# Optimization experiments

Measured on AMD Instinct MI355X. Metric: run time of the kernel, lower is better.

## Reference

```python
import jax, jax.numpy as jnp
import numpy as np

LEVELS = 3  # num_basis = 1 + 1 + 2 + 4 = 8


def _haar_basis(x):
    """Closed-form vectorized Haar basis, x: [B, F] raw inputs.

    Replaces the original nested per-feature/per-level/per-bucket mask loops:
    at each level only one bucket k = floor(u*freq) is active, with value
    +2^(level/2) on the left half of the bucket and -2^(level/2) on the right
    half (x == 1.0 falls in the right half of the last bucket, matching the
    torch edge-case handling).
    """
    u = (jnp.tanh(x) + 1.0) / 2.0  # normalize to [0, 1]
    cols = [jnp.ones_like(u)[..., None]]  # scaling function phi
    for level in range(LEVELS):
        freq = 2 ** level
        k = jnp.clip(jnp.floor(u * freq), 0, freq - 1).astype(jnp.int32)  # bucket idx
        mid = (k.astype(u.dtype) + 0.5) / freq
        amp = jnp.asarray(2.0 ** (level / 2), u.dtype)
        sign = jnp.where(u < mid, amp, -amp)  # [B, F]
        cols.append(jax.nn.one_hot(k, freq, dtype=u.dtype) * sign[..., None])
    return jnp.concatenate(cols, axis=-1)  # [B, F, num_basis]


def setup_inputs() -> dict:
    key = jax.random.key(0)
    k1, k2, k3 = jax.random.split(key, 3)
    B, F, O, NB = 32768, 1024, 64, 8
    x = jax.random.normal(k1, (B, F), dtype=jnp.float32)
    coeffs = jax.random.normal(k2, (F, O, NB), dtype=jnp.float32) * 0.05
    base_weight = jax.random.normal(k3, (F, O), dtype=jnp.float32) * 0.05
    return {"x": x, "coeffs": coeffs, "base_weight": base_weight}


def reference(x, coeffs, base_weight):
    basis = _haar_basis(x)                         # [B, F, NB]
    wave_out = jnp.einsum('bin,ion->bo', basis, coeffs)  # [B, O]
    out = wave_out + x @ base_weight               # residual path
    kl = jnp.zeros((1,), dtype=x.dtype)            # non-variational: kl = 0
    return (out, kl)
```

## Files before the change

### kernel.cpp

```cpp
#include <hip/hip_runtime.h>
#include <math.h>


typedef __attribute__((ext_vector_type(8))) short short8;
typedef __attribute__((ext_vector_type(4))) float f32x4;

__device__ __forceinline__ unsigned int f2bf(float f) {
  unsigned int u = __float_as_uint(f);
  u += 0x7FFFu + ((u >> 16) & 1u);
  return u >> 16;
}

__device__ __forceinline__ void gen_basis(int j, unsigned int* d) {
  d[0] = (j < 4) ? 0x3F803F80u : 0xBF803F80u;
  unsigned int sq1 = (j & 2) ? 0xBFB5u : 0x3FB5u;
  d[1] = (j & 4) ? (sq1 << 16) : sq1;
  unsigned long long sd2 = (j & 1) ? 0xC000ull : 0x4000ull;
  unsigned long long d23 = sd2 << ((j & 6) << 3);
  d[2] = (unsigned int)d23;
  d[3] = (unsigned int)(d23 >> 32);
}

#define BARRIER() __asm__ volatile("s_waitcnt lgkmcnt(0)\n\ts_barrier" ::: "memory")

__device__ __forceinline__ void build_chunk(const float4& xa, const float4& xb,
                                            uint4* __restrict__ dst) {
  float xv[8];
  xv[0] = xa.x; xv[1] = xa.y; xv[2] = xa.z; xv[3] = xa.w;
  xv[4] = xb.x; xv[5] = xb.y; xv[6] = xb.z; xv[7] = xb.w;
  float t8v[8];
  unsigned int bad = 0;
#pragma unroll
  for (int ff = 0; ff < 8; ++ff) {
    float e = __expf(2.0f * xv[ff]);
    float r = __builtin_amdgcn_rcpf(e + 1.0f);
    float t8 = __builtin_fmaf(-8.0f, r, 8.0f);
    float rn = rintf(t8);
    if (fabsf(t8 - rn) < 3e-5f) bad |= 1u << ff;
    t8v[ff] = t8;
  }
  if (__builtin_expect(bad != 0, 0)) {
#pragma unroll
    for (int ff = 0; ff < 8; ++ff)
      if (bad & (1u << ff)) {
        float tf = (float)tanh((double)xv[ff]);
        t8v[ff] = ((tf + 1.0f) * 0.5f) * 8.0f;
      }
  }
  unsigned int dw[36];
#pragma unroll
  for (int p = 0; p < 4; ++p) {
    int je = (int)t8v[2 * p];     je = je > 7 ? 7 : je;
    int jo = (int)t8v[2 * p + 1]; jo = jo > 7 ? 7 : jo;
    gen_basis(je, &dw[9 * p]);
    dw[9 * p + 4] = f2bf(xv[2 * p]) | (f2bf(xv[2 * p + 1]) << 16);
    gen_basis(jo, &dw[9 * p + 5]);
  }
#pragma unroll
  for (int gg = 0; gg < 9; ++gg) {
    uint4 qv; qv.x = dw[4 * gg]; qv.y = dw[4 * gg + 1];
    qv.z = dw[4 * gg + 2]; qv.w = dw[4 * gg + 3];
    dst[gg * 256] = qv;
  }
}

__global__ __launch_bounds__(256) void build_w(const float* __restrict__ coeffs,
                                               const float* __restrict__ bw,
                                               uint4* __restrict__ Wsw) {
  const int l = threadIdx.x & 63;
  const int t = threadIdx.x >> 6;
  const int g = blockIdx.x;
  const int c = g / 9, j = g - c * 9;
  const int R = c * 4 + (l >> 4);
  const int o = t * 16 + (l & 15);
  unsigned int dwv[4];
#pragma unroll
  for (int jj = 0; jj < 8; ++jj) {
    int d = 8 * j + jj;
    int p = d / 18;
    int e = d - p * 18;
    int f, n;
    if (e < 8)       { f = 8 * R + 2 * p;     n = e; }
    else if (e == 8) { f = 8 * R + 2 * p;     n = 8; }
    else if (e == 9) { f = 8 * R + 2 * p + 1; n = 8; }
    else             { f = 8 * R + 2 * p + 1; n = e - 10; }
    float v = (n < 8) ? coeffs[(f * 64 + o) * 8 + n] : bw[f * 64 + o];
    unsigned int h = f2bf(v);
    if (jj & 1) dwv[jj >> 1] |= h << 16; else dwv[jj >> 1] = h;
  }
  uint4 qq; qq.x = dwv[0]; qq.y = dwv[1]; qq.z = dwv[2]; qq.w = dwv[3];
  Wsw[(g * 4 + t) * 64 + l] = qq;
}

template <int NS>
__device__ __forceinline__ void run_main(const float* __restrict__ xrow,
                                         const uint4* __restrict__ Wsw,
                                         uint4* __restrict__ Albuf,
                                         f32x4* acc,
                                         int s0, int q, int mm, int bdoff, int l) {
  float4 xa = *(const float4*)(xrow);
  float4 xb = *(const float4*)(xrow + 4);
  build_chunk(xa, xb, Albuf + bdoff);
  xa = *(const float4*)(xrow + 32);
  xb = *(const float4*)(xrow + 36);
  BARRIER();
  for (int c = 0; c < 32; ++c) {
    uint4* cur = Albuf + (c & 1) * 2304;
    uint4* nxt = Albuf + ((c + 1) & 1) * 2304;
    uint4 Bv[NS][4];
#pragma unroll
    for (int i = 0; i < NS; ++i) {
      const uint4* wp = Wsw + (size_t)((c * 9 + s0 + 4 * i) * 256) + l;
      Bv[i][0] = wp[0]; Bv[i][1] = wp[64]; Bv[i][2] = wp[128]; Bv[i][3] = wp[192];
    }
    if (c + 1 < 32) {
      build_chunk(xa, xb, nxt + bdoff);
      if (c + 2 < 32) {
        xa = *(const float4*)(xrow + (c + 2) * 32);
        xb = *(const float4*)(xrow + (c + 2) * 32 + 4);
      }
    }
#pragma unroll
    for (int i = 0; i < NS; ++i) {
      const int sl = s0 + 4 * i;
      const uint4* rb = cur + sl * 256 + q * 64 + mm;
      short8 a0 = __builtin_bit_cast(short8, rb[0]);
      short8 a1 = __builtin_bit_cast(short8, rb[16]);
      short8 a2 = __builtin_bit_cast(short8, rb[32]);
      short8 a3 = __builtin_bit_cast(short8, rb[48]);
#pragma unroll
      for (int t = 0; t < 4; ++t) {
        short8 Bt = __builtin_bit_cast(short8, Bv[i][t]);
        acc[0 * 4 + t] = __builtin_amdgcn_mfma_f32_16x16x32_bf16(a0, Bt, acc[0 * 4 + t], 0, 0, 0);
        acc[1 * 4 + t] = __builtin_amdgcn_mfma_f32_16x16x32_bf16(a1, Bt, acc[1 * 4 + t], 0, 0, 0);
        acc[2 * 4 + t] = __builtin_amdgcn_mfma_f32_16x16x32_bf16(a2, Bt, acc[2 * 4 + t], 0, 0, 0);
        acc[3 * 4 + t] = __builtin_amdgcn_mfma_f32_16x16x32_bf16(a3, Bt, acc[3 * 4 + t], 0, 0, 0);
      }
    }
    BARRIER();
  }
}

__global__ __launch_bounds__(256, 2) void wavelet_gemm(const float* __restrict__ x,
                                                       const uint4* __restrict__ Wsw,
                                                       float* __restrict__ out,
                                                       int out_size) {
  __shared__ uint4 Albuf[2 * 9 * 4 * 64];
  const int tid = threadIdx.x;
  const int l = tid & 63;
  const int w = tid >> 6;
  const int q = l >> 4;
  const int mm = l & 15;
  const int m = tid & 63;
  const int bdoff = w * 64 + m;
  const long rowbase = (long)blockIdx.x * 64;

  f32x4 acc[16];
#pragma unroll
  for (int i = 0; i < 16; ++i) acc[i] = (f32x4){0.f, 0.f, 0.f, 0.f};

  const float* xrow = x + (rowbase + m) * 1024 + w * 8;

  if (w == 0) run_main<3>(xrow, Wsw, Albuf, acc, 0, q, mm, bdoff, l);
  else        run_main<2>(xrow, Wsw, Albuf, acc, w, q, mm, bdoff, l);

  float* P = (float*)Albuf;
  float* W = P + w * 4096;
#pragma unroll
  for (int rt = 0; rt < 4; ++rt)
#pragma unroll
    for (int tt = 0; tt < 4; ++tt)
      *(f32x4*)(W + (16 * tt + mm) * 64 + 16 * rt + 4 * q) = acc[rt * 4 + tt];
  BARRIER();

  const int col = tid & 63;
  float* og = out + (size_t)rowbase * 64;
#pragma unroll
  for (int s = 0; s < 4; ++s) {
    int rg = s * 4 + (tid >> 6);
    f32x4 v = *(f32x4*)(P + 0 * 4096 + col * 64 + 4 * rg);
    v = v + *(f32x4*)(P + 1 * 4096 + col * 64 + 4 * rg);
    v = v + *(f32x4*)(P + 2 * 4096 + col * 64 + 4 * rg);
    v = v + *(f32x4*)(P + 3 * 4096 + col * 64 + 4 * rg);
#pragma unroll
    for (int r = 0; r < 4; ++r)
      og[(4 * rg + r) * 64 + col] = v[r];
  }
  if (blockIdx.x == 0 && tid == 0) out[out_size - 1] = 0.0f;
}

extern "C" void kernel_launch(void* const* d_in, const int* in_sizes, int n_in,
                              void* d_out, int out_size, void* d_ws, size_t ws_size,
                              hipStream_t stream) {
  const float* x      = (const float*)d_in[0];
  const float* coeffs = (const float*)d_in[1];
  const float* bw     = (const float*)d_in[2];
  uint4* Wsw = (uint4*)d_ws;
  float* out = (float*)d_out;

  build_w<<<288, 256, 0, stream>>>(coeffs, bw, Wsw);
  wavelet_gemm<<<512, 256, 0, stream>>>(x, (const uint4*)Wsw, out, out_size);
}
```

Measured before the change: 231.7 us.

## Split GEMM tile across 8 waves by output quadrant, dropping split-K LDS reduction

The main kernel now uses 512 threads (8 waves). Each wave owns a 32-row by 16-column output tile and covers the full K range, instead of 4 waves splitting K and reducing partial sums through shared memory. Basis building is halved per thread, so each thread encodes 4 features, and results are written directly from accumulators. This removes the LDS reduction and the heavy per-wave accumulator state, at the cost of each wave loading all 9 B slices per chunk and issuing fewer MFMAs per A load.

```diff
diff --git a/kernel.cpp b/kernel.cpp
--- a/kernel.cpp
+++ b/kernel.cpp
@@ -23,15 +23,13 @@
 
 #define BARRIER() __asm__ volatile("s_waitcnt lgkmcnt(0)\n\ts_barrier" ::: "memory")
 
-__device__ __forceinline__ void build_chunk(const float4& xa, const float4& xb,
-                                            uint4* __restrict__ dst) {
-  float xv[8];
-  xv[0] = xa.x; xv[1] = xa.y; xv[2] = xa.z; xv[3] = xa.w;
-  xv[4] = xb.x; xv[5] = xb.y; xv[6] = xb.z; xv[7] = xb.w;
-  float t8v[8];
+__device__ __forceinline__ void build_half(const float4& xq,
+                                           uint4* __restrict__ dst, int h) {
+  float xv[4] = {xq.x, xq.y, xq.z, xq.w};
+  float t8v[4];
   unsigned int bad = 0;
 #pragma unroll
-  for (int ff = 0; ff < 8; ++ff) {
+  for (int ff = 0; ff < 4; ++ff) {
     float e = __expf(2.0f * xv[ff]);
     float r = __builtin_amdgcn_rcpf(e + 1.0f);
     float t8 = __builtin_fmaf(-8.0f, r, 8.0f);
@@ -41,27 +39,34 @@
   }
   if (__builtin_expect(bad != 0, 0)) {
 #pragma unroll
-    for (int ff = 0; ff < 8; ++ff)
+    for (int ff = 0; ff < 4; ++ff)
       if (bad & (1u << ff)) {
         float tf = (float)tanh((double)xv[ff]);
         t8v[ff] = ((tf + 1.0f) * 0.5f) * 8.0f;
       }
   }
-  unsigned int dw[36];
+  unsigned int dw[18];
 #pragma unroll
-  for (int p = 0; p < 4; ++p) {
+  for (int p = 0; p < 2; ++p) {
     int je = (int)t8v[2 * p];     je = je > 7 ? 7 : je;
     int jo = (int)t8v[2 * p + 1]; jo = jo > 7 ? 7 : jo;
     gen_basis(je, &dw[9 * p]);
     dw[9 * p + 4] = f2bf(xv[2 * p]) | (f2bf(xv[2 * p + 1]) << 16);
     gen_basis(jo, &dw[9 * p + 5]);
   }
+  const int db = h ? 2 : 0;
+  const int gb = h ? 5 : 0;
 #pragma unroll
-  for (int gg = 0; gg < 9; ++gg) {
-    uint4 qv; qv.x = dw[4 * gg]; qv.y = dw[4 * gg + 1];
-    qv.z = dw[4 * gg + 2]; qv.w = dw[4 * gg + 3];
-    dst[gg * 256] = qv;
+  for (int k = 0; k < 4; ++k) {
+    uint4 qv;
+    qv.x = dw[db + 4 * k];     qv.y = dw[db + 4 * k + 1];
+    qv.z = dw[db + 4 * k + 2]; qv.w = dw[db + 4 * k + 3];
+    dst[(gb + k) * 256] = qv;
   }
+  uint2 hv;
+  if (h) { hv.x = dw[0];  hv.y = dw[1];  }
+  else   { hv.x = dw[16]; hv.y = dw[17]; }
+  ((uint2*)(dst + 4 * 256))[h] = hv;
 }
 
 __global__ __launch_bounds__(256) void build_w(const float* __restrict__ coeffs,
@@ -85,107 +90,73 @@
     else if (e == 9) { f = 8 * R + 2 * p + 1; n = 8; }
     else             { f = 8 * R + 2 * p + 1; n = e - 10; }
     float v = (n < 8) ? coeffs[(f * 64 + o) * 8 + n] : bw[f * 64 + o];
-    unsigned int h = f2bf(v);
-    if (jj & 1) dwv[jj >> 1] |= h << 16; else dwv[jj >> 1] = h;
+    unsigned int hh = f2bf(v);
+    if (jj & 1) dwv[jj >> 1] |= hh << 16; else dwv[jj >> 1] = hh;
   }
   uint4 qq; qq.x = dwv[0]; qq.y = dwv[1]; qq.z = dwv[2]; qq.w = dwv[3];
   Wsw[(g * 4 + t) * 64 + l] = qq;
 }
 
-template <int NS>
-__device__ __forceinline__ void run_main(const float* __restrict__ xrow,
-                                         const uint4* __restrict__ Wsw,
-                                         uint4* __restrict__ Albuf,
-                                         f32x4* acc,
-                                         int s0, int q, int mm, int bdoff, int l) {
-  float4 xa = *(const float4*)(xrow);
-  float4 xb = *(const float4*)(xrow + 4);
-  build_chunk(xa, xb, Albuf + bdoff);
-  xa = *(const float4*)(xrow + 32);
-  xb = *(const float4*)(xrow + 36);
-  BARRIER();
-  for (int c = 0; c < 32; ++c) {
-    uint4* cur = Albuf + (c & 1) * 2304;
-    uint4* nxt = Albuf + ((c + 1) & 1) * 2304;
-    uint4 Bv[NS][4];
-#pragma unroll
-    for (int i = 0; i < NS; ++i) {
-      const uint4* wp = Wsw + (size_t)((c * 9 + s0 + 4 * i) * 256) + l;
-      Bv[i][0] = wp[0]; Bv[i][1] = wp[64]; Bv[i][2] = wp[128]; Bv[i][3] = wp[192];
-    }
-    if (c + 1 < 32) {
-      build_chunk(xa, xb, nxt + bdoff);
-      if (c + 2 < 32) {
-        xa = *(const float4*)(xrow + (c + 2) * 32);
-        xb = *(const float4*)(xrow + (c + 2) * 32 + 4);
-      }
-    }
-#pragma unroll
-    for (int i = 0; i < NS; ++i) {
-      const int sl = s0 + 4 * i;
-      const uint4* rb = cur + sl * 256 + q * 64 + mm;
-      short8 a0 = __builtin_bit_cast(short8, rb[0]);
-      short8 a1 = __builtin_bit_cast(short8, rb[16]);
-      short8 a2 = __builtin_bit_cast(short8, rb[32]);
-      short8 a3 = __builtin_bit_cast(short8, rb[48]);
-#pragma unroll
-      for (int t = 0; t < 4; ++t) {
-        short8 Bt = __builtin_bit_cast(short8, Bv[i][t]);
-        acc[0 * 4 + t] = __builtin_amdgcn_mfma_f32_16x16x32_bf16(a0, Bt, acc[0 * 4 + t], 0, 0, 0);
-        acc[1 * 4 + t] = __builtin_amdgcn_mfma_f32_16x16x32_bf16(a1, Bt, acc[1 * 4 + t], 0, 0, 0);
-        acc[2 * 4 + t] = __builtin_amdgcn_mfma_f32_16x16x32_bf16(a2, Bt, acc[2 * 4 + t], 0, 0, 0);
-        acc[3 * 4 + t] = __builtin_amdgcn_mfma_f32_16x16x32_bf16(a3, Bt, acc[3 * 4 + t], 0, 0, 0);
-      }
-    }
-    BARRIER();
-  }
-}
-
-__global__ __launch_bounds__(256, 2) void wavelet_gemm(const float* __restrict__ x,
+__global__ __launch_bounds__(512, 4) void wavelet_gemm(const float* __restrict__ x,
                                                        const uint4* __restrict__ Wsw,
                                                        float* __restrict__ out,
                                                        int out_size) {
-  __shared__ uint4 Albuf[2 * 9 * 4 * 64];
+  __shared__ uint4 Albuf[2 * 9 * 256];
   const int tid = threadIdx.x;
   const int l = tid & 63;
   const int w = tid >> 6;
   const int q = l >> 4;
   const int mm = l & 15;
-  const int m = tid & 63;
-  const int bdoff = w * 64 + m;
+  const int mh = w >> 2;
+  const int nq = w & 3;
+  const int r = w & 3;
+  const int h = w >> 2;
+  const int m = l;
   const long rowbase = (long)blockIdx.x * 64;
 
-  f32x4 acc[16];
-#pragma unroll
-  for (int i = 0; i < 16; ++i) acc[i] = (f32x4){0.f, 0.f, 0.f, 0.f};
+  const int wr_off  = r * 64 + m;
+  const int rd_base = q * 64 + mh * 32 + mm;
 
-  const float* xrow = x + (rowbase + m) * 1024 + w * 8;
+  f32x4 acc0 = (f32x4){0.f, 0.f, 0.f, 0.f};
+  f32x4 acc1 = (f32x4){0.f, 0.f, 0.f, 0.f};
 
-  if (w == 0) run_main<3>(xrow, Wsw, Albuf, acc, 0, q, mm, bdoff, l);
-  else        run_main<2>(xrow, Wsw, Albuf, acc, w, q, mm, bdoff, l);
+  const float* xrow = x + (rowbase + m) * 1024 + r * 8 + h * 4;
 
-  float* P = (float*)Albuf;
-  float* W = P + w * 4096;
-#pragma unroll
-  for (int rt = 0; rt < 4; ++rt)
-#pragma unroll
-    for (int tt = 0; tt < 4; ++tt)
-      *(f32x4*)(W + (16 * tt + mm) * 64 + 16 * rt + 4 * q) = acc[rt * 4 + tt];
+  float4 xa = *(const float4*)(xrow);
+  build_half(xa, Albuf + wr_off, h);
+  xa = *(const float4*)(xrow + 32);
   BARRIER();
 
-  const int col = tid & 63;
+  for (int c = 0; c < 32; ++c) {
+    uint4* cur = Albuf + (c & 1) * 2304;
+    uint4* nxt = Albuf + ((c + 1) & 1) * 2304;
+    uint4 Bv[9];
+#pragma unroll
+    for (int s = 0; s < 9; ++s)
+      Bv[s] = Wsw[((c * 9 + s) * 4 + nq) * 64 + l];
+    if (c + 1 < 32) {
+      build_half(xa, nxt + wr_off, h);
+      if (c + 2 < 32) xa = *(const float4*)(xrow + (c + 2) * 32);
+    }
+#pragma unroll
+    for (int s = 0; s < 9; ++s) {
+      const uint4* rb = cur + s * 256 + rd_base;
+      short8 a0 = __builtin_bit_cast(short8, rb[0]);
+      short8 a1 = __builtin_bit_cast(short8, rb[16]);
+      short8 Bt = __builtin_bit_cast(short8, Bv[s]);
+      acc0 = __builtin_amdgcn_mfma_f32_16x16x32_bf16(a0, Bt, acc0, 0, 0, 0);
+      acc1 = __builtin_amdgcn_mfma_f32_16x16x32_bf16(a1, Bt, acc1, 0, 0, 0);
+    }
+    BARRIER();
+  }
+
   float* og = out + (size_t)rowbase * 64;
+  const int col  = nq * 16 + mm;
+  const int row0 = mh * 32 + q * 4;
 #pragma unroll
-  for (int s = 0; s < 4; ++s) {
-    int rg = s * 4 + (tid >> 6);
-    f32x4 v = *(f32x4*)(P + 0 * 4096 + col * 64 + 4 * rg);
-    v = v + *(f32x4*)(P + 1 * 4096 + col * 64 + 4 * rg);
-    v = v + *(f32x4*)(P + 2 * 4096 + col * 64 + 4 * rg);
-    v = v + *(f32x4*)(P + 3 * 4096 + col * 64 + 4 * rg);
+  for (int j = 0; j < 4; ++j) og[(row0 + j) * 64 + col] = acc0[j];
 #pragma unroll
-    for (int r = 0; r < 4; ++r)
-      og[(4 * rg + r) * 64 + col] = v[r];
-  }
+  for (int j = 0; j < 4; ++j) og[(row0 + 16 + j) * 64 + col] = acc1[j];
   if (blockIdx.x == 0 && tid == 0) out[out_size - 1] = 0.0f;
 }
 
@@ -199,5 +170,5 @@
   float* out = (float*)d_out;
 
   build_w<<<288, 256, 0, stream>>>(coeffs, bw, Wsw);
-  wavelet_gemm<<<512, 256, 0, stream>>>(x, (const uint4*)Wsw, out, out_size);
+  wavelet_gemm<<<512, 512, 0, stream>>>(x, (const uint4*)Wsw, out, out_size);
 }
```

Result: slower. 240.9 us (+4.0%).
